# Performance work log

Hardware: AMD Instinct MI355X
Metric: run time of the kernel (lower is better)

## Reference

```python
import jax, jax.numpy as jnp
import numpy as np

H = 6  # num_heads
D = 384  # embedding_dim


def _rot(seg, coord):
    # seg: [BN, H, T, L], coord: [BN, T]; rotate interleaved even/odd pairs
    L = seg.shape[-1]
    pairs = max(L // 2, 1)
    inv_freq = 1.0 / (10000.0 ** (jnp.arange(pairs, dtype=seg.dtype) / pairs))
    ang = coord[..., None] * inv_freq          # [BN, T, pairs]
    cos = jnp.cos(ang)[:, None]                # [BN, 1, T, pairs]
    sin = jnp.sin(ang)[:, None]
    even, odd = seg[..., 0::2], seg[..., 1::2]
    re = even * cos - odd * sin
    ro = even * sin + odd * cos
    return jnp.stack((re, ro), axis=-1).reshape(seg.shape)


def _apply_rope3(t, pos, chunk):
    # t: [BN, H, T, Hd], pos: [BN, T, 3]; three axis chunks, tail untouched
    parts, s = [], 0
    for i in range(3):
        parts.append(_rot(t[..., s:s + chunk], pos[..., i]))
        s += chunk
    parts.append(t[..., s:])
    return jnp.concatenate(parts, axis=-1)


def setup_inputs() -> dict:
    key = jax.random.key(0)
    ks = jax.random.split(key, 10)
    B, N, T = 8, 64, 128
    scale = 1.0 / np.sqrt(D)
    return {
        "padded_batches": jax.random.normal(ks[0], (B, N, T, D), jnp.float32),
        "sum_token": jax.random.normal(ks[1], (B, N, 1, D), jnp.float32),
        "positions_3d": jax.random.uniform(ks[2], (B, N, T, 3), jnp.float32),
        "Wq": jax.random.normal(ks[3], (D, D), jnp.float32) * scale,
        "bq": jax.random.normal(ks[4], (D,), jnp.float32) * scale,
        "Wk": jax.random.normal(ks[5], (D, D), jnp.float32) * scale,
        "bk": jax.random.normal(ks[6], (D,), jnp.float32) * scale,
        "Wv": jax.random.normal(ks[7], (D, D), jnp.float32) * scale,
        "bv": jax.random.normal(ks[8], (D,), jnp.float32) * scale,
        "masks": jax.random.randint(ks[9], (B, N, T), 0, 2, jnp.int32),
    }


def reference(padded_batches, sum_token, positions_3d, Wq, bq, Wk, bk, Wv, bv, masks):
    B, N, T, Dm = padded_batches.shape
    Hd = Dm // H
    chunk = Hd // 6 * 2

    # masked mean-pool summary token (summary_mode='avg')
    w = masks[..., None].astype(padded_batches.dtype)          # [B,N,T,1]
    denom = jnp.clip(w.sum(axis=-2, keepdims=True), 1e-6, None)
    summary = (padded_batches * w).sum(axis=-2, keepdims=True) / denom  # [B,N,1,D]

    q = (padded_batches @ Wq + bq).reshape(B * N, T, H, Hd).transpose(0, 2, 1, 3)  # [BN,H,T,Hd]
    k = (summary @ Wk + bk).reshape(B * N, 1, H, Hd).transpose(0, 2, 1, 3)         # [BN,H,1,Hd]
    v = (summary @ Wv + bv).reshape(B * N, 1, H, Hd).transpose(0, 2, 1, 3)

    # 3-axis RoPE on q (token positions) and k (pooled positions)
    pos_summary = (positions_3d * w).sum(axis=-2, keepdims=True) / denom  # [B,N,1,3]
    pos_q = positions_3d.reshape(B * N, T, 3)
    pos_k = pos_summary.reshape(B * N, 1, 3)
    q = _apply_rope3(q, pos_q, chunk)
    k = _apply_rope3(k, pos_k, chunk)

    # SDPA with T queries vs 1 key
    scores = jnp.einsum('bhtd,bhkd->bhtk', q, k) / np.float32(np.sqrt(Hd))  # [BN,H,T,1]
    mask_add = jnp.where(masks.reshape(B * N, 1, T, 1) == 0,
                         jnp.finfo(jnp.float32).min, 0.0)
    attn_w = jax.nn.softmax(scores + mask_add, axis=-1)
    attn = jnp.einsum('bhtk,bhkd->bhtd', attn_w, v)  # [BN,H,T,Hd]

    out = attn.transpose(0, 2, 1, 3).reshape(B, N, T, Dm) + padded_batches
    return out
```

## Files before the change

kernel.cpp:

```cpp
#include <hip/hip_runtime.h>
#include <hip/hip_bf16.h>


#define DM 384
#define TT 128
#define C4 96
#define RG 8
#define NT (C4 * RG)

__global__ __launch_bounds__(NT) void gmha_v3_kernel(
    const float* __restrict__ padded,
    const float* __restrict__ Wv,
    const float* __restrict__ bv,
    const int*   __restrict__ masks,
    float*       __restrict__ out)
{
    const int bn = blockIdx.x;
    const int t  = threadIdx.x;
    const int c  = t % C4;
    const int r  = t / C4;

    __shared__ float  w_sh[TT];
    __shared__ float4 part_sh[RG][C4];
    __shared__ float  summ_sh[DM];
    __shared__ float4 v_sh[C4];

    const float4* __restrict__ p4 = (const float4*)(padded + (size_t)bn * TT * DM);
    float4*       __restrict__ o4 = (float4*)(out    + (size_t)bn * TT * DM);

    if (t < TT) w_sh[t] = (float)masks[bn * TT + t];
    __syncthreads();

    float4 acc = make_float4(0.f, 0.f, 0.f, 0.f);
    #pragma unroll
    for (int i = 0; i < TT / RG; ++i) {
        const int    tt = r + i * RG;
        const float  w  = w_sh[tt];
        const float4 x  = p4[tt * C4 + c];
        acc.x += x.x * w; acc.y += x.y * w; acc.z += x.z * w; acc.w += x.w * w;
    }
    part_sh[r][c] = acc;
    __syncthreads();

    if (t < C4) {
        float wsum = 0.f;
        #pragma unroll
        for (int i = 0; i < TT; ++i) wsum += w_sh[i];
        const float inv_denom = 1.0f / fmaxf(wsum, 1e-6f);
        float4 s = make_float4(0.f, 0.f, 0.f, 0.f);
        #pragma unroll
        for (int g = 0; g < RG; ++g) {
            const float4 a = part_sh[g][t];
            s.x += a.x; s.y += a.y; s.z += a.z; s.w += a.w;
        }
        s.x *= inv_denom; s.y *= inv_denom; s.z *= inv_denom; s.w *= inv_denom;
        ((float4*)summ_sh)[t] = s;
    }
    __syncthreads();

    float4 vacc = make_float4(0.f, 0.f, 0.f, 0.f);
    const int e0 = r * (DM / RG);
    #pragma unroll 8
    for (int i = 0; i < DM / RG; ++i) {
        const int   e  = e0 + i;
        const float se = summ_sh[e];
        const float4 wv = *(const float4*)(Wv + (size_t)e * DM + 4 * c);
        vacc.x += se * wv.x; vacc.y += se * wv.y;
        vacc.z += se * wv.z; vacc.w += se * wv.w;
    }
    part_sh[r][c] = vacc;
    __syncthreads();

    if (t < C4) {
        float4 v = ((const float4*)bv)[t];
        #pragma unroll
        for (int g = 0; g < RG; ++g) {
            const float4 a = part_sh[g][t];
            v.x += a.x; v.y += a.y; v.z += a.z; v.w += a.w;
        }
        v_sh[t] = v;
    }
    __syncthreads();

    const float4 v = v_sh[c];
    #pragma unroll
    for (int i = 0; i < TT / RG; ++i) {
        const int tt = r + i * RG;
        float4 x = p4[tt * C4 + c];
        x.x += v.x; x.y += v.y; x.z += v.z; x.w += v.w;
        o4[tt * C4 + c] = x;
    }
}

extern "C" void kernel_launch(void* const* d_in, const int* in_sizes, int n_in,
                              void* d_out, int out_size, void* d_ws, size_t ws_size,
                              hipStream_t stream) {
    const float* padded = (const float*)d_in[0];
    const float* Wv     = (const float*)d_in[7];
    const float* bv     = (const float*)d_in[8];
    const int*   masks  = (const int*)d_in[9];
    float* out = (float*)d_out;

    const int BN = 8 * 64;
    gmha_v3_kernel<<<BN, NT, 0, stream>>>(padded, Wv, bv, masks, out);
}
```

Measured before the change: 223.8 us.

## Split fused kernel into partial-sum, batched matvec, and broadcast-add kernels

Replaces the single per-row kernel with three launches: masked partial sums over half-rows, a matvec that processes two rows per block to share Wv loads, and a separate residual-add pass over quarter-rows. The aim is more blocks in flight and less serialized work per block. In exchange the input tensor is read in a separate kernel from the add pass, losing on-chip locality, and two extra launches plus workspace traffic are added.

New measurement: 222.3 us. About the same (-0.7%).

```diff
diff --git a/kernel.cpp b/kernel.cpp
--- a/kernel.cpp
+++ b/kernel.cpp
@@ -5,36 +5,32 @@
 #define DM 384
 #define TT 128
 #define C4 96
-#define RG 8
-#define NT (C4 * RG)
+#define BN_TOT 512
 
-__global__ __launch_bounds__(NT) void gmha_v3_kernel(
+__global__ __launch_bounds__(384) void k1_partial_sums(
     const float* __restrict__ padded,
-    const float* __restrict__ Wv,
-    const float* __restrict__ bv,
     const int*   __restrict__ masks,
-    float*       __restrict__ out)
+    float*       __restrict__ ws_part)
 {
-    const int bn = blockIdx.x;
-    const int t  = threadIdx.x;
-    const int c  = t % C4;
-    const int r  = t / C4;
+    const int bn   = blockIdx.x >> 1;
+    const int half = blockIdx.x & 1;
+    const int t = threadIdx.x;
+    const int c = t % C4;
+    const int r = t / C4;
 
-    __shared__ float  w_sh[TT];
-    __shared__ float4 part_sh[RG][C4];
-    __shared__ float  summ_sh[DM];
-    __shared__ float4 v_sh[C4];
+    __shared__ float  w_sh[64];
+    __shared__ float4 part_sh[4][C4];
 
-    const float4* __restrict__ p4 = (const float4*)(padded + (size_t)bn * TT * DM);
-    float4*       __restrict__ o4 = (float4*)(out    + (size_t)bn * TT * DM);
+    if (t < 64) w_sh[t] = (float)masks[bn * TT + half * 64 + t];
+    __syncthreads();
 
-    if (t < TT) w_sh[t] = (float)masks[bn * TT + t];
-    __syncthreads();
+    const float4* __restrict__ p4 =
+        (const float4*)(padded + (size_t)bn * TT * DM) + half * 64 * C4;
 
     float4 acc = make_float4(0.f, 0.f, 0.f, 0.f);
     #pragma unroll
-    for (int i = 0; i < TT / RG; ++i) {
-        const int    tt = r + i * RG;
+    for (int i = 0; i < 16; ++i) {
+        const int    tt = r + i * 4;
         const float  w  = w_sh[tt];
         const float4 x  = p4[tt * C4 + c];
         acc.x += x.x * w; acc.y += x.y * w; acc.z += x.z * w; acc.w += x.w * w;
@@ -43,49 +39,111 @@
     __syncthreads();
 
     if (t < C4) {
-        float wsum = 0.f;
+        const float4 a0 = part_sh[0][t], a1 = part_sh[1][t];
+        const float4 a2 = part_sh[2][t], a3 = part_sh[3][t];
+        float4 s;
+        s.x = a0.x + a1.x + a2.x + a3.x;
+        s.y = a0.y + a1.y + a2.y + a3.y;
+        s.z = a0.z + a1.z + a2.z + a3.z;
+        s.w = a0.w + a1.w + a2.w + a3.w;
+        ((float4*)(ws_part + ((size_t)bn * 2 + half) * DM))[t] = s;
+    }
+}
+
+__global__ __launch_bounds__(384) void k2_matvec(
+    const float* __restrict__ ws_part,
+    const int*   __restrict__ masks,
+    const float* __restrict__ Wv,
+    const float* __restrict__ bv,
+    float*       __restrict__ ws_v)
+{
+    const int bn0 = blockIdx.x * 2;
+    const int bn1 = bn0 + 1;
+    const int t = threadIdx.x;
+    const int c = t % C4;
+    const int r = t / C4;
+
+    __shared__ float summ0[DM], summ1[DM];
+    __shared__ float4 part0[4][C4], part1[4][C4];
+    __shared__ float w0_sh[TT], w1_sh[TT];
+
+    if (t < TT) w0_sh[t] = (float)masks[bn0 * TT + t];
+    else if (t < 2 * TT) w1_sh[t - TT] = (float)masks[bn1 * TT + (t - TT)];
+    __syncthreads();
+
+    if (t < C4) {
+        float ws0 = 0.f, ws1 = 0.f;
         #pragma unroll
-        for (int i = 0; i < TT; ++i) wsum += w_sh[i];
-        const float inv_denom = 1.0f / fmaxf(wsum, 1e-6f);
-        float4 s = make_float4(0.f, 0.f, 0.f, 0.f);
-        #pragma unroll
-        for (int g = 0; g < RG; ++g) {
-            const float4 a = part_sh[g][t];
-            s.x += a.x; s.y += a.y; s.z += a.z; s.w += a.w;
-        }
-        s.x *= inv_denom; s.y *= inv_denom; s.z *= inv_denom; s.w *= inv_denom;
-        ((float4*)summ_sh)[t] = s;
+        for (int i = 0; i < TT; ++i) { ws0 += w0_sh[i]; ws1 += w1_sh[i]; }
+        const float id0 = 1.0f / fmaxf(ws0, 1e-6f);
+        const float id1 = 1.0f / fmaxf(ws1, 1e-6f);
+        const float4 p00 = ((const float4*)(ws_part + (size_t)bn0 * 2 * DM))[t];
+        const float4 p01 = ((const float4*)(ws_part + ((size_t)bn0 * 2 + 1) * DM))[t];
+        const float4 p10 = ((const float4*)(ws_part + (size_t)bn1 * 2 * DM))[t];
+        const float4 p11 = ((const float4*)(ws_part + ((size_t)bn1 * 2 + 1) * DM))[t];
+        float4 s0, s1;
+        s0.x = (p00.x + p01.x) * id0; s0.y = (p00.y + p01.y) * id0;
+        s0.z = (p00.z + p01.z) * id0; s0.w = (p00.w + p01.w) * id0;
+        s1.x = (p10.x + p11.x) * id1; s1.y = (p10.y + p11.y) * id1;
+        s1.z = (p10.z + p11.z) * id1; s1.w = (p10.w + p11.w) * id1;
+        ((float4*)summ0)[t] = s0;
+        ((float4*)summ1)[t] = s1;
     }
     __syncthreads();
 
-    float4 vacc = make_float4(0.f, 0.f, 0.f, 0.f);
-    const int e0 = r * (DM / RG);
+    float4 a0 = make_float4(0.f, 0.f, 0.f, 0.f);
+    float4 a1 = make_float4(0.f, 0.f, 0.f, 0.f);
+    const int e0 = r * C4;
     #pragma unroll 8
-    for (int i = 0; i < DM / RG; ++i) {
+    for (int i = 0; i < C4; ++i) {
         const int   e  = e0 + i;
-        const float se = summ_sh[e];
+        const float s0 = summ0[e];
+        const float s1 = summ1[e];
         const float4 wv = *(const float4*)(Wv + (size_t)e * DM + 4 * c);
-        vacc.x += se * wv.x; vacc.y += se * wv.y;
-        vacc.z += se * wv.z; vacc.w += se * wv.w;
+        a0.x += s0 * wv.x; a0.y += s0 * wv.y; a0.z += s0 * wv.z; a0.w += s0 * wv.w;
+        a1.x += s1 * wv.x; a1.y += s1 * wv.y; a1.z += s1 * wv.z; a1.w += s1 * wv.w;
     }
-    part_sh[r][c] = vacc;
+    part0[r][c] = a0;
+    part1[r][c] = a1;
     __syncthreads();
 
     if (t < C4) {
-        float4 v = ((const float4*)bv)[t];
+        const float4 b = ((const float4*)bv)[t];
+        float4 v0 = b, v1 = b;
         #pragma unroll
-        for (int g = 0; g < RG; ++g) {
-            const float4 a = part_sh[g][t];
-            v.x += a.x; v.y += a.y; v.z += a.z; v.w += a.w;
+        for (int g = 0; g < 4; ++g) {
+            const float4 q0 = part0[g][t], q1 = part1[g][t];
+            v0.x += q0.x; v0.y += q0.y; v0.z += q0.z; v0.w += q0.w;
+            v1.x += q1.x; v1.y += q1.y; v1.z += q1.z; v1.w += q1.w;
         }
-        v_sh[t] = v;
+        ((float4*)(ws_v + (size_t)bn0 * DM))[t] = v0;
+        ((float4*)(ws_v + (size_t)bn1 * DM))[t] = v1;
     }
+}
+
+__global__ __launch_bounds__(384) void k3_add(
+    const float* __restrict__ padded,
+    const float* __restrict__ ws_v,
+    float*       __restrict__ out)
+{
+    const int bn = blockIdx.x >> 2;
+    const int q  = blockIdx.x & 3;
+    const int t = threadIdx.x;
+    const int c = t % C4;
+    const int r = t / C4;
+
+    __shared__ float4 v_sh[C4];
+    if (t < C4) v_sh[t] = ((const float4*)(ws_v + (size_t)bn * DM))[t];
     __syncthreads();
+
+    const size_t base = (size_t)bn * TT * C4 + (size_t)q * 32 * C4;
+    const float4* __restrict__ p4 = (const float4*)padded + base;
+    float4*       __restrict__ o4 = (float4*)out + base;
 
     const float4 v = v_sh[c];
     #pragma unroll
-    for (int i = 0; i < TT / RG; ++i) {
-        const int tt = r + i * RG;
+    for (int i = 0; i < 8; ++i) {
+        const int tt = r + i * 4;
         float4 x = p4[tt * C4 + c];
         x.x += v.x; x.y += v.y; x.z += v.z; x.w += v.w;
         o4[tt * C4 + c] = x;
@@ -101,6 +159,10 @@
     const int*   masks  = (const int*)d_in[9];
     float* out = (float*)d_out;
 
-    const int BN = 8 * 64;
-    gmha_v3_kernel<<<BN, NT, 0, stream>>>(padded, Wv, bv, masks, out);
+    float* ws_part = (float*)d_ws;
+    float* ws_v    = ws_part + (size_t)BN_TOT * 2 * DM;
+
+    k1_partial_sums<<<BN_TOT * 2, 384, 0, stream>>>(padded, masks, ws_part);
+    k2_matvec<<<BN_TOT / 2, 384, 0, stream>>>(ws_part, masks, Wv, bv, ws_v);
+    k3_add<<<BN_TOT * 4, 384, 0, stream>>>(padded, ws_v, out);
 }
```
